# Performance work log

Hardware: AMD Instinct MI355X
Metric: run time of the kernel (lower is better)

## Reference

```python
import jax, jax.numpy as jnp
import numpy as np

IN_FEATURES = 1024
N_CLASSES = 50257
CUTOFFS = [0, 5000, 20000, 50257]  # cluster boundaries (lows/highs)


def setup_inputs() -> dict:
    key = jax.random.key(0)
    ks = jax.random.split(key, 6)
    tokens = jax.random.randint(ks[0], (8, 4096), 0, N_CLASSES, dtype=jnp.int32)
    scale = 0.02
    head_emb = jax.random.normal(ks[1], (5000, IN_FEATURES), jnp.float32) * scale
    # tail cluster 0: hsz = 1024 // 2 = 512, osz = 20000 - 5000 = 15000
    tail0_emb = jax.random.normal(ks[2], (15000, 512), jnp.float32) * scale
    tail0_w = jax.random.normal(ks[3], (IN_FEATURES, 512), jnp.float32) * scale  # torch Linear weight (out, in)
    # tail cluster 1: hsz = 1024 // 4 = 256, osz = 50257 - 20000 = 30257
    tail1_emb = jax.random.normal(ks[4], (30257, 256), jnp.float32) * scale
    tail1_w = jax.random.normal(ks[5], (IN_FEATURES, 256), jnp.float32) * scale
    return {"tokens": tokens, "head_emb": head_emb, "tail0_emb": tail0_emb,
            "tail0_w": tail0_w, "tail1_emb": tail1_emb, "tail1_w": tail1_w}


def reference(tokens, head_emb, tail0_emb, tail0_w, tail1_emb, tail1_w):
    # AdaptiveInput forward (eval mode: Dropout = identity).
    # Each token id falls in exactly one cluster [low, high); lookup in that
    # cluster's table (shifted by low), project tails to in_features, scatter
    # back. We express gather+scatter as masked adds (clusters are disjoint).
    B, S = tokens.shape
    t = tokens.reshape(-1)  # [N]

    def cluster_out(low, high, table, w=None):
        mask = ((t >= low) & (t < high))[:, None]                 # [N, 1]
        idx = jnp.clip(t - low, 0, table.shape[0] - 1)            # in-range gather
        e = table[idx]                                            # [N, hsz]
        if w is not None:
            e = e @ w.T                                           # [N, in_features]
        return jnp.where(mask, e, jnp.zeros((), e.dtype))

    out = cluster_out(CUTOFFS[0], CUTOFFS[1], head_emb)
    out = out + cluster_out(CUTOFFS[1], CUTOFFS[2], tail0_emb, tail0_w)
    out = out + cluster_out(CUTOFFS[2], CUTOFFS[3], tail1_emb, tail1_w)
    return out.reshape(B, S, IN_FEATURES)
```

## Files before the change

### kernel.cpp

```cpp
#include <hip/hip_runtime.h>
#include <hip/hip_bf16.h>


typedef __attribute__((ext_vector_type(8))) short short8;
typedef __attribute__((ext_vector_type(4))) float f32x4;
typedef unsigned int u32;

__device__ __forceinline__ u32 pk2bf(float a, float b) {
    __hip_bfloat162 h = __float22bfloat162_rn(make_float2(a, b));
    union { __hip_bfloat162 h; u32 u; } c; c.h = h; return c.u;
}

__device__ __forceinline__ void glds16(const void* g, void* l) {
    __builtin_amdgcn_global_load_lds((const __attribute__((address_space(1))) u32*)g,
                                     (__attribute__((address_space(3))) u32*)l, 16, 0, 0);
}

__global__ __launch_bounds__(256) void ai_prep(const float* __restrict__ w0, const float* __restrict__ w1,
                                               unsigned short* __restrict__ o0, unsigned short* __restrict__ o1,
                                               int* __restrict__ cnt, int do_cvt) {
    if (blockIdx.x == 0 && threadIdx.x < 8) cnt[threadIdx.x] = 0;
    if (!do_cvt) return;
    int i = blockIdx.x * blockDim.x + threadIdx.x;
    const float* src; unsigned short* dst; int base;
    if (i < 65536) { src = w0; dst = o0; base = i * 8; }
    else           { src = w1; dst = o1; base = (i - 65536) * 8; }
    float4 a = *(const float4*)(src + base);
    float4 b = *(const float4*)(src + base + 4);
    uint4 q = { pk2bf(a.x, a.y), pk2bf(a.z, a.w), pk2bf(b.x, b.y), pk2bf(b.z, b.w) };
    *(uint4*)(dst + base) = q;
}

__global__ __launch_bounds__(256) void ai_partition(const int* __restrict__ tokens, int n,
                                                    int* __restrict__ cnt,
                                                    int* __restrict__ l0, int* __restrict__ l1) {
    __shared__ int wcnt[4][3];
    __shared__ int wbase[4][3];
    int i = blockIdx.x * blockDim.x + threadIdx.x;
    int lane = threadIdx.x & 63, w = threadIdx.x >> 6;
    int t = (i < n) ? tokens[i] : -1;
    int c = (t < 0) ? 3 : (t >= 20000) ? 1 : (t >= 5000) ? 0 : 2;
    unsigned long long m0 = __ballot(c == 0);
    unsigned long long m1 = __ballot(c == 1);
    unsigned long long m2 = __ballot(c == 2);
    if (lane == 0) { wcnt[w][0] = __popcll(m0); wcnt[w][1] = __popcll(m1); wcnt[w][2] = __popcll(m2); }
    __syncthreads();
    if (threadIdx.x < 3) {
        int j = threadIdx.x;
        int s0 = wcnt[0][j], s1 = wcnt[1][j], s2 = wcnt[2][j], s3 = wcnt[3][j];
        int base = atomicAdd(&cnt[j], s0 + s1 + s2 + s3);
        wbase[0][j] = base; wbase[1][j] = base + s0;
        wbase[2][j] = base + s0 + s1; wbase[3][j] = base + s0 + s1 + s2;
    }
    __syncthreads();
    unsigned long long lt = (1ull << lane) - 1ull;
    if (c == 0)      l0[wbase[w][0] + __popcll(m0 & lt)] = i;
    else if (c == 1) l1[wbase[w][1] + __popcll(m1 & lt)] = i;
    else if (c == 2) l1[n - 1 - (wbase[w][2] + __popcll(m2 & lt))] = i;
}

__global__ __launch_bounds__(256) void ai_head_copy(const int* __restrict__ tokens,
                                                    const int* __restrict__ l1, int n,
                                                    const int* __restrict__ cnt,
                                                    const float* __restrict__ emb,
                                                    float* __restrict__ out) {
    const int hc = cnt[2];
    for (int m = blockIdx.x; m < hc; m += gridDim.x) {
        int p = l1[n - 1 - m];
        int t = tokens[p];
        const float4* src = (const float4*)(emb + (size_t)t * 1024);
        float4* dst = (float4*)(out + (size_t)p * 1024);
        dst[threadIdx.x] = src[threadIdx.x];
    }
}

template<bool PRE>
__global__ __launch_bounds__(256) void ai_tail_gemm(
    const int* __restrict__ tokens,
    const int* __restrict__ l0, const int* __restrict__ l1,
    const int* __restrict__ cnt,
    const float* __restrict__ emb0, const float* __restrict__ emb1,
    const float* __restrict__ w0f, const float* __restrict__ w1f,
    const unsigned short* __restrict__ w0b, const unsigned short* __restrict__ w1b,
    float* __restrict__ out)
{
    constexpr int BK = 64;
    constexpr int LDKA = 72;
    __shared__ __align__(16) unsigned short As[128 * LDKA];
    __shared__ __align__(16) unsigned short Bs[2][128 * BK];
    __shared__ int s_erow[128];
    __shared__ int s_opos[128];

    const int z = blockIdx.z;
    const int K     = z ? 256 : 512;
    const int low   = z ? 20000 : 5000;
    const int count = cnt[z];
    const int* list = z ? l1 : l0;
    const float* emb = z ? emb1 : emb0;
    const float* wf  = z ? w1f : w0f;
    const unsigned short* wb = z ? w1b : w0b;

    const int m0 = blockIdx.y * 128;
    if (m0 >= count) return;
    const int n0 = blockIdx.x * 128;
    const int tid = threadIdx.x;

    if (tid < 128) {
        int m = m0 + tid;
        if (m < count) {
            int p = list[m];
            s_opos[tid] = p;
            s_erow[tid] = tokens[p] - low;
        } else {
            s_opos[tid] = -1;
            s_erow[tid] = -1;
        }
    }
    __syncthreads();

    f32x4 acc[4][4];
    #pragma unroll
    for (int i = 0; i < 4; i++)
        #pragma unroll
        for (int j = 0; j < 4; j++)
            acc[i][j] = (f32x4){0.f, 0.f, 0.f, 0.f};

    const int lane = tid & 63;
    const int wave = tid >> 6;
    const int wm = (wave >> 1) * 64;
    const int wn = (wave & 1) * 64;
    const int fr = lane & 15;
    const int fk = (lane >> 4) * 8;
    const int swzm = (fr & 7) << 4;

    const int srow  = tid >> 1;
    const int shalf = tid & 1;
    const int er = s_erow[srow];

    const int rlc  = lane >> 3;
    const int c16s = (lane & 7) ^ rlc;

    float4 areg[8];
    float4 breg[8];

    auto loadA = [&](int kt) {
        if (er >= 0) {
            const float4* src = (const float4*)(emb + (size_t)er * K + kt + shalf * 32);
            #pragma unroll
            for (int j = 0; j < 8; j++) areg[j] = src[j];
        }
    };
    auto writeA = [&]() {
        unsigned short* dst = &As[srow * LDKA + shalf * 32];
        if (er >= 0) {
            #pragma unroll
            for (int j = 0; j < 4; j++) {
                uint4 q = { pk2bf(areg[2*j].x, areg[2*j].y), pk2bf(areg[2*j].z, areg[2*j].w),
                            pk2bf(areg[2*j+1].x, areg[2*j+1].y), pk2bf(areg[2*j+1].z, areg[2*j+1].w) };
                *(uint4*)(dst + j * 8) = q;
            }
        } else {
            uint4 zq = {0u, 0u, 0u, 0u};
            #pragma unroll
            for (int j = 0; j < 4; j++) *(uint4*)(dst + j * 8) = zq;
        }
    };
    auto issueB = [&](int kt, int buf) {
        if (PRE) {
            #pragma unroll
            for (int i = 0; i < 4; i++) {
                int chunk = wave * 4 + i;
                const unsigned short* src = wb + (size_t)(n0 + chunk * 8 + rlc) * K + kt + c16s * 8;
                glds16(src, &Bs[buf][chunk * 512]);
            }
        } else {
            const float4* src = (const float4*)(wf + (size_t)(n0 + srow) * K + kt + shalf * 32);
            #pragma unroll
            for (int j = 0; j < 8; j++) breg[j] = src[j];
        }
    };
    auto writeB = [&](int buf) {
        if (!PRE) {
            char* base = (char*)&Bs[buf][0] + srow * 128;
            int sm = (srow & 7) << 4;
            #pragma unroll
            for (int j = 0; j < 4; j++) {
                uint4 q = { pk2bf(breg[2*j].x, breg[2*j].y), pk2bf(breg[2*j].z, breg[2*j].w),
                            pk2bf(breg[2*j+1].x, breg[2*j+1].y), pk2bf(breg[2*j+1].z, breg[2*j+1].w) };
                *(uint4*)(base + ((shalf * 64 + j * 16) ^ sm)) = q;
            }
        }
    };

    auto compute = [&](int buf) {
        const char* Bbase = (const char*)&Bs[buf][0];
        #pragma unroll
        for (int kk = 0; kk < BK; kk += 32) {
            short8 af[4], bf[4];
            #pragma unroll
            for (int f = 0; f < 4; f++) {
                af[f] = *(const short8*)&As[(wm + f * 16 + fr) * LDKA + kk + fk];
                int rb = wn + f * 16 + fr;
                bf[f] = *(const short8*)(Bbase + rb * 128 + (((kk + fk) << 1) ^ swzm));
            }
            #pragma unroll
            for (int i = 0; i < 4; i++)
                #pragma unroll
                for (int j = 0; j < 4; j++)
                    acc[i][j] = __builtin_amdgcn_mfma_f32_16x16x32_bf16(af[i], bf[j], acc[i][j], 0, 0, 0);
        }
    };

    issueB(0, 0);
    loadA(0);
    writeA();
    writeB(0);
    __syncthreads();

    const int nt = K / BK;
    for (int t = 0; t < nt; t++) {
        const int cur = t & 1;
        const bool more = (t + 1 < nt);
        if (more) {
            issueB((t + 1) * BK, cur ^ 1);
            loadA((t + 1) * BK);
        }
        compute(cur);
        __syncthreads();
        if (more) {
            writeA();
            writeB(cur ^ 1);
            __syncthreads();
        }
    }

    const int rbase = (lane >> 4) * 4;
    #pragma unroll
    for (int i = 0; i < 4; i++) {
        #pragma unroll
        for (int r = 0; r < 4; r++) {
            int ml = wm + i * 16 + rbase + r;
            if (m0 + ml < count) {
                float* orow = out + (size_t)s_opos[ml] * 1024 + n0 + wn + fr;
                orow[0]  = acc[i][0][r];
                orow[16] = acc[i][1][r];
                orow[32] = acc[i][2][r];
                orow[48] = acc[i][3][r];
            }
        }
    }
}

extern "C" void kernel_launch(void* const* d_in, const int* in_sizes, int n_in,
                              void* d_out, int out_size, void* d_ws, size_t ws_size,
                              hipStream_t stream) {
    const int*   tokens   = (const int*)d_in[0];
    const float* head_emb = (const float*)d_in[1];
    const float* t0_emb   = (const float*)d_in[2];
    const float* t0_w     = (const float*)d_in[3];
    const float* t1_emb   = (const float*)d_in[4];
    const float* t1_w     = (const float*)d_in[5];
    float* out = (float*)d_out;
    const int N = in_sizes[0];

    int* cnt = (int*)d_ws;
    int* l0  = cnt + 16;
    int* l1  = l0 + N;
    size_t base_need = 64 + (size_t)2 * N * 4;
    size_t wbf_elems = (size_t)1024 * 512 + (size_t)1024 * 256;
    bool pre = ws_size >= base_need + wbf_elems * 2;
    unsigned short* wbf0 = (unsigned short*)((char*)d_ws + base_need);
    unsigned short* wbf1 = wbf0 + (size_t)1024 * 512;

    ai_prep<<<384, 256, 0, stream>>>(t0_w, t1_w, wbf0, wbf1, cnt, pre ? 1 : 0);
    ai_partition<<<(N + 255) / 256, 256, 0, stream>>>(tokens, N, cnt, l0, l1);
    ai_head_copy<<<1024, 256, 0, stream>>>(tokens, l1, N, cnt, head_emb, out);

    dim3 g(8, (N + 127) / 128, 2);
    if (pre)
        ai_tail_gemm<true><<<g, 256, 0, stream>>>(tokens, l0, l1, cnt, t0_emb, t1_emb,
                                                  t0_w, t1_w, wbf0, wbf1, out);
    else
        ai_tail_gemm<false><<<g, 256, 0, stream>>>(tokens, l0, l1, cnt, t0_emb, t1_emb,
                                                   t0_w, t1_w, wbf0, wbf1, out);
}
```

Before: 268.9 us.

## Pre-convert tail embedding tables to bf16 and stream A tiles via direct-to-LDS loads

The prep kernel now converts both tail embedding tables to bf16 along with the projection weights, using a grid-stride loop over four source/destination pairs. The tail GEMM then loads gathered A rows with global_load_lds into a double-buffered, XOR-swizzled LDS tile, matching the B path, and drops the second barrier per k-step in the pre-converted path. Block indices are also remapped so neighbouring M tiles land on the same XCD. The aim is to remove the fp32 register load and convert step from the GEMM inner loop. The cost is converting roughly 15M table elements on every call, which adds a large read and write pass.

```diff
diff --git a/kernel.cpp b/kernel.cpp
--- a/kernel.cpp
+++ b/kernel.cpp
@@ -5,6 +5,7 @@
 typedef __attribute__((ext_vector_type(8))) short short8;
 typedef __attribute__((ext_vector_type(4))) float f32x4;
 typedef unsigned int u32;
+typedef unsigned short u16;
 
 __device__ __forceinline__ u32 pk2bf(float a, float b) {
     __hip_bfloat162 h = __float22bfloat162_rn(make_float2(a, b));
@@ -16,19 +17,29 @@
                                      (__attribute__((address_space(3))) u32*)l, 16, 0, 0);
 }
 
-__global__ __launch_bounds__(256) void ai_prep(const float* __restrict__ w0, const float* __restrict__ w1,
-                                               unsigned short* __restrict__ o0, unsigned short* __restrict__ o1,
-                                               int* __restrict__ cnt, int do_cvt) {
+__global__ __launch_bounds__(256) void ai_prep(
+    const float* __restrict__ s0, const float* __restrict__ s1,
+    const float* __restrict__ s2, const float* __restrict__ s3,
+    u16* __restrict__ d0, u16* __restrict__ d1,
+    u16* __restrict__ d2, u16* __restrict__ d3,
+    int c0, int c1, int c2, int c3,
+    int* __restrict__ cnt, int do_cvt)
+{
     if (blockIdx.x == 0 && threadIdx.x < 8) cnt[threadIdx.x] = 0;
     if (!do_cvt) return;
-    int i = blockIdx.x * blockDim.x + threadIdx.x;
-    const float* src; unsigned short* dst; int base;
-    if (i < 65536) { src = w0; dst = o0; base = i * 8; }
-    else           { src = w1; dst = o1; base = (i - 65536) * 8; }
-    float4 a = *(const float4*)(src + base);
-    float4 b = *(const float4*)(src + base + 4);
-    uint4 q = { pk2bf(a.x, a.y), pk2bf(a.z, a.w), pk2bf(b.x, b.y), pk2bf(b.z, b.w) };
-    *(uint4*)(dst + base) = q;
+    int total = c0 + c1 + c2 + c3;
+    for (int i = blockIdx.x * blockDim.x + threadIdx.x; i < total;
+         i += gridDim.x * blockDim.x) {
+        const float* s; u16* d; int j = i;
+        if (j < c0)              { s = s0; d = d0; }
+        else if ((j -= c0) < c1) { s = s1; d = d1; }
+        else if ((j -= c1) < c2) { s = s2; d = d2; }
+        else          { j -= c2;   s = s3; d = d3; }
+        float4 a = *(const float4*)(s + (size_t)j * 8);
+        float4 b = *(const float4*)(s + (size_t)j * 8 + 4);
+        uint4 q = { pk2bf(a.x, a.y), pk2bf(a.z, a.w), pk2bf(b.x, b.y), pk2bf(b.z, b.w) };
+        *(uint4*)(d + (size_t)j * 8) = q;
+    }
 }
 
 __global__ __launch_bounds__(256) void ai_partition(const int* __restrict__ tokens, int n,
@@ -79,15 +90,15 @@
     const int* __restrict__ tokens,
     const int* __restrict__ l0, const int* __restrict__ l1,
     const int* __restrict__ cnt,
-    const float* __restrict__ emb0, const float* __restrict__ emb1,
+    const float* __restrict__ e0f, const float* __restrict__ e1f,
     const float* __restrict__ w0f, const float* __restrict__ w1f,
-    const unsigned short* __restrict__ w0b, const unsigned short* __restrict__ w1b,
+    const u16* __restrict__ e0b, const u16* __restrict__ e1b,
+    const u16* __restrict__ w0b, const u16* __restrict__ w1b,
     float* __restrict__ out)
 {
     constexpr int BK = 64;
-    constexpr int LDKA = 72;
-    __shared__ __align__(16) unsigned short As[128 * LDKA];
-    __shared__ __align__(16) unsigned short Bs[2][128 * BK];
+    __shared__ __align__(16) u16 As[2][128 * BK];
+    __shared__ __align__(16) u16 Bs[2][128 * BK];
     __shared__ int s_erow[128];
     __shared__ int s_opos[128];
 
@@ -96,13 +107,16 @@
     const int low   = z ? 20000 : 5000;
     const int count = cnt[z];
     const int* list = z ? l1 : l0;
-    const float* emb = z ? emb1 : emb0;
-    const float* wf  = z ? w1f : w0f;
-    const unsigned short* wb = z ? w1b : w0b;
-
-    const int m0 = blockIdx.y * 128;
+    const float* ef = z ? e1f : e0f;
+    const float* wf = z ? w1f : w0f;
+    const u16*   eb = z ? e1b : e0b;
+    const u16*   wb = z ? w1b : w0b;
+
+    const int id = blockIdx.y * 8 + blockIdx.x;
+    const int xcd = id & 7, q = id >> 3;
+    const int m0 = (((q >> 3) << 3) | xcd) * 128;
+    const int n0 = (q & 7) * 128;
     if (m0 >= count) return;
-    const int n0 = blockIdx.x * 128;
     const int tid = threadIdx.x;
 
     if (tid < 128) {
@@ -133,75 +147,78 @@
     const int fk = (lane >> 4) * 8;
     const int swzm = (fr & 7) << 4;
 
+    const int rlc  = lane >> 3;
+    const int c16s = (lane & 7) ^ rlc;
+
+    const u16* aSrc[4];
+    const u16* bSrc[4];
+    if (PRE) {
+        #pragma unroll
+        for (int i = 0; i < 4; i++) {
+            int row = (wave * 4 + i) * 8 + rlc;
+            int er = s_erow[row]; if (er < 0) er = 0;
+            aSrc[i] = eb + (size_t)er * K + c16s * 8;
+            bSrc[i] = wb + (size_t)(n0 + row) * K + c16s * 8;
+        }
+    }
+
     const int srow  = tid >> 1;
     const int shalf = tid & 1;
-    const int er = s_erow[srow];
-
-    const int rlc  = lane >> 3;
-    const int c16s = (lane & 7) ^ rlc;
-
-    float4 areg[8];
-    float4 breg[8];
-
-    auto loadA = [&](int kt) {
-        if (er >= 0) {
-            const float4* src = (const float4*)(emb + (size_t)er * K + kt + shalf * 32);
-            #pragma unroll
-            for (int j = 0; j < 8; j++) areg[j] = src[j];
-        }
-    };
-    auto writeA = [&]() {
-        unsigned short* dst = &As[srow * LDKA + shalf * 32];
-        if (er >= 0) {
-            #pragma unroll
-            for (int j = 0; j < 4; j++) {
-                uint4 q = { pk2bf(areg[2*j].x, areg[2*j].y), pk2bf(areg[2*j].z, areg[2*j].w),
-                            pk2bf(areg[2*j+1].x, areg[2*j+1].y), pk2bf(areg[2*j+1].z, areg[2*j+1].w) };
-                *(uint4*)(dst + j * 8) = q;
-            }
-        } else {
-            uint4 zq = {0u, 0u, 0u, 0u};
-            #pragma unroll
-            for (int j = 0; j < 4; j++) *(uint4*)(dst + j * 8) = zq;
-        }
-    };
-    auto issueB = [&](int kt, int buf) {
+    const int er32 = s_erow[srow];
+    float4 areg[8], breg[8];
+
+    auto issue = [&](int kt, int buf) {
         if (PRE) {
             #pragma unroll
             for (int i = 0; i < 4; i++) {
                 int chunk = wave * 4 + i;
-                const unsigned short* src = wb + (size_t)(n0 + chunk * 8 + rlc) * K + kt + c16s * 8;
-                glds16(src, &Bs[buf][chunk * 512]);
+                glds16(aSrc[i] + kt, &As[buf][chunk * 512]);
+                glds16(bSrc[i] + kt, &Bs[buf][chunk * 512]);
             }
         } else {
-            const float4* src = (const float4*)(wf + (size_t)(n0 + srow) * K + kt + shalf * 32);
-            #pragma unroll
-            for (int j = 0; j < 8; j++) breg[j] = src[j];
+            if (er32 >= 0) {
+                const float4* src = (const float4*)(ef + (size_t)er32 * K + kt + shalf * 32);
+                #pragma unroll
+                for (int j = 0; j < 8; j++) areg[j] = src[j];
+            }
+            const float4* srcB = (const float4*)(wf + (size_t)(n0 + srow) * K + kt + shalf * 32);
+            #pragma unroll
+            for (int j = 0; j < 8; j++) breg[j] = srcB[j];
         }
     };
-    auto writeB = [&](int buf) {
+    auto publish = [&](int buf) {
         if (!PRE) {
-            char* base = (char*)&Bs[buf][0] + srow * 128;
             int sm = (srow & 7) << 4;
+            char* baseA = (char*)&As[buf][0] + srow * 128;
+            char* baseB = (char*)&Bs[buf][0] + srow * 128;
             #pragma unroll
             for (int j = 0; j < 4; j++) {
-                uint4 q = { pk2bf(breg[2*j].x, breg[2*j].y), pk2bf(breg[2*j].z, breg[2*j].w),
-                            pk2bf(breg[2*j+1].x, breg[2*j+1].y), pk2bf(breg[2*j+1].z, breg[2*j+1].w) };
-                *(uint4*)(base + ((shalf * 64 + j * 16) ^ sm)) = q;
+                uint4 qa;
+                if (er32 >= 0)
+                    qa = (uint4){ pk2bf(areg[2*j].x, areg[2*j].y), pk2bf(areg[2*j].z, areg[2*j].w),
+                                  pk2bf(areg[2*j+1].x, areg[2*j+1].y), pk2bf(areg[2*j+1].z, areg[2*j+1].w) };
+                else qa = (uint4){0u, 0u, 0u, 0u};
+                uint4 qb = { pk2bf(breg[2*j].x, breg[2*j].y), pk2bf(breg[2*j].z, breg[2*j].w),
+                             pk2bf(breg[2*j+1].x, breg[2*j+1].y), pk2bf(breg[2*j+1].z, breg[2*j+1].w) };
+                *(uint4*)(baseA + ((shalf * 64 + j * 16) ^ sm)) = qa;
+                *(uint4*)(baseB + ((shalf * 64 + j * 16) ^ sm)) = qb;
             }
         }
     };
 
     auto compute = [&](int buf) {
+        const char* Abase = (const char*)&As[buf][0];
         const char* Bbase = (const char*)&Bs[buf][0];
         #pragma unroll
         for (int kk = 0; kk < BK; kk += 32) {
             short8 af[4], bf[4];
             #pragma unroll
             for (int f = 0; f < 4; f++) {
-                af[f] = *(const short8*)&As[(wm + f * 16 + fr) * LDKA + kk + fk];
+                int ra = wm + f * 16 + fr;
                 int rb = wn + f * 16 + fr;
-                bf[f] = *(const short8*)(Bbase + rb * 128 + (((kk + fk) << 1) ^ swzm));
+                int cb = ((kk + fk) << 1);
+                af[f] = *(const short8*)(Abase + ra * 128 + (cb ^ ((ra & 7) << 4)));
+                bf[f] = *(const short8*)(Bbase + rb * 128 + (cb ^ ((rb & 7) << 4)));
             }
             #pragma unroll
             for (int i = 0; i < 4; i++)
@@ -211,26 +228,20 @@
         }
     };
 
-    issueB(0, 0);
-    loadA(0);
-    writeA();
-    writeB(0);
+    issue(0, 0);
+    publish(0);
     __syncthreads();
 
     const int nt = K / BK;
     for (int t = 0; t < nt; t++) {
         const int cur = t & 1;
         const bool more = (t + 1 < nt);
-        if (more) {
-            issueB((t + 1) * BK, cur ^ 1);
-            loadA((t + 1) * BK);
-        }
+        if (more) issue((t + 1) * BK, cur ^ 1);
         compute(cur);
         __syncthreads();
         if (more) {
-            writeA();
-            writeB(cur ^ 1);
-            __syncthreads();
+            publish(cur ^ 1);
+            if (!PRE) __syncthreads();
         }
     }
 
@@ -262,25 +273,36 @@
     const float* t1_w     = (const float*)d_in[5];
     float* out = (float*)d_out;
     const int N = in_sizes[0];
+    const int nE0 = in_sizes[2];
+    const int nW0 = in_sizes[3];
+    const int nE1 = in_sizes[4];
+    const int nW1 = in_sizes[5];
 
     int* cnt = (int*)d_ws;
     int* l0  = cnt + 16;
     int* l1  = l0 + N;
     size_t base_need = 64 + (size_t)2 * N * 4;
-    size_t wbf_elems = (size_t)1024 * 512 + (size_t)1024 * 256;
-    bool pre = ws_size >= base_need + wbf_elems * 2;
-    unsigned short* wbf0 = (unsigned short*)((char*)d_ws + base_need);
-    unsigned short* wbf1 = wbf0 + (size_t)1024 * 512;
-
-    ai_prep<<<384, 256, 0, stream>>>(t0_w, t1_w, wbf0, wbf1, cnt, pre ? 1 : 0);
+    size_t tbl_elems = (size_t)nW0 + nW1 + nE0 + nE1;
+    bool pre = ws_size >= base_need + tbl_elems * 2;
+    u16* wb0 = (u16*)((char*)d_ws + base_need);
+    u16* wb1 = wb0 + nW0;
+    u16* eb0 = wb1 + nW1;
+    u16* eb1 = eb0 + nE0;
+
+    ai_prep<<<2048, 256, 0, stream>>>(t0_w, t1_w, t0_emb, t1_emb,
+                                      wb0, wb1, eb0, eb1,
+                                      nW0 / 8, nW1 / 8, nE0 / 8, nE1 / 8,
+                                      cnt, pre ? 1 : 0);
     ai_partition<<<(N + 255) / 256, 256, 0, stream>>>(tokens, N, cnt, l0, l1);
     ai_head_copy<<<1024, 256, 0, stream>>>(tokens, l1, N, cnt, head_emb, out);
 
     dim3 g(8, (N + 127) / 128, 2);
     if (pre)
-        ai_tail_gemm<true><<<g, 256, 0, stream>>>(tokens, l0, l1, cnt, t0_emb, t1_emb,
-                                                  t0_w, t1_w, wbf0, wbf1, out);
+        ai_tail_gemm<true><<<g, 256, 0, stream>>>(tokens, l0, l1, cnt,
+                                                  t0_emb, t1_emb, t0_w, t1_w,
+                                                  eb0, eb1, wb0, wb1, out);
     else
-        ai_tail_gemm<false><<<g, 256, 0, stream>>>(tokens, l0, l1, cnt, t0_emb, t1_emb,
-                                                   t0_w, t1_w, wbf0, wbf1, out);
-}
+        ai_tail_gemm<false><<<g, 256, 0, stream>>>(tokens, l0, l1, cnt,
+                                                   t0_emb, t1_emb, t0_w, t1_w,
+                                                   eb0, eb1, wb0, wb1, out);
+}
```

Result: faster. 250.7 us (-6.8%).
